# Kernel tuning notes

Measured on AMD Instinct MI355X. Metric: run time of the kernel, lower is better.

The kernel has to match this reference:

```python
import jax, jax.numpy as jnp
import numpy as np

B, L, E, H = 64, 512, 128, 256


def setup_inputs() -> dict:
    key = jax.random.key(0)
    ks = jax.random.split(key, 16)
    s = 0.05
    return {
        "embedded_inputs": jax.random.normal(ks[0], (B, L, E), jnp.float32),
        "decoder_input": jax.random.normal(ks[1], (B, E), jnp.float32),
        "h0": jax.random.normal(ks[2], (B, H), jnp.float32),
        "c0": jax.random.normal(ks[3], (B, H), jnp.float32),
        "context": jax.random.normal(ks[4], (B, L, H), jnp.float32),
        # LSTM cell params
        "Wi": jax.random.normal(ks[5], (4 * H, E), jnp.float32) * s,
        "bi": jnp.zeros((4 * H,), jnp.float32),
        "Wh": jax.random.normal(ks[6], (4 * H, H), jnp.float32) * s,
        "bh": jnp.zeros((4 * H,), jnp.float32),
        # hidden_out: Linear(2H -> H)
        "Wo": jax.random.normal(ks[7], (H, 2 * H), jnp.float32) * s,
        "bo": jnp.zeros((H,), jnp.float32),
        # attention params: input_linear(H->H), context conv1d(H->H,k=1), V [H]
        "Wa_in": jax.random.normal(ks[8], (H, H), jnp.float32) * s,
        "ba_in": jnp.zeros((H,), jnp.float32),
        "Wa_ctx": jax.random.normal(ks[9], (H, H), jnp.float32) * s,
        "ba_ctx": jnp.zeros((H,), jnp.float32),
        "V": jax.random.normal(ks[10], (H,), jnp.float32) * s,
    }


def reference(embedded_inputs, decoder_input, h0, c0, context,
              Wi, bi, Wh, bh, Wo, bo, Wa_in, ba_in, Wa_ctx, ba_ctx, V):
    # Precompute projected context once (Conv1d with kernel 1 == per-position linear): [B,L,H]
    ctx_proj = jnp.einsum('blh,gh->blg', context, Wa_ctx) + ba_ctx

    def step(carry, _):
        dec_in, h, c, mask = carry
        gates = dec_in @ Wi.T + bi + h @ Wh.T + bh              # [B,4H]
        i_g, f_g, g_g, o_g = jnp.split(gates, 4, axis=1)
        i_g = jax.nn.sigmoid(i_g)
        f_g = jax.nn.sigmoid(f_g)
        g_g = jnp.tanh(g_g)
        o_g = jax.nn.sigmoid(o_g)
        c_t = f_g * c + i_g * g_g
        h_t = o_g * jnp.tanh(c_t)
        # attention
        inp = h_t @ Wa_in.T + ba_in                              # [B,H]
        scores = jnp.einsum('h,blh->bl', V, jnp.tanh(inp[:, None, :] + ctx_proj))
        scores = jnp.where(mask == 0, -jnp.inf, scores)
        alpha = jax.nn.softmax(scores, axis=1)                   # [B,L]
        att_hidden = jnp.einsum('bl,blh->bh', alpha, ctx_proj)
        hidden_t = jnp.tanh(jnp.concatenate([att_hidden, h_t], axis=1) @ Wo.T + bo)
        # pointer: argmax over still-available positions
        masked_outs = alpha * mask
        idx = jnp.argmax(masked_outs, axis=1)                    # [B]
        one_hot = jax.nn.one_hot(idx, L, dtype=mask.dtype)
        mask_next = mask * (1.0 - one_hot)
        dec_next = jnp.take_along_axis(embedded_inputs, idx[:, None, None], axis=1)[:, 0]
        return (dec_next, hidden_t, c_t, mask_next), (alpha, idx)

    mask0 = jnp.ones((B, L), jnp.float32)
    carry0 = (decoder_input, h0, c0, mask0)
    (dec_f, h_f, c_f, _), (alphas, ptrs) = jax.lax.scan(step, carry0, None, length=L)
    outputs = jnp.transpose(alphas, (1, 0, 2))                   # [B,L,L]
    pointers = jnp.transpose(ptrs, (1, 0))                       # [B,L]
    return outputs, pointers, h_f, c_f
```

## Files before the change

kernel.cpp:

```cpp
#include <hip/hip_runtime.h>
#include <math.h>

#define SCOPE __HIP_MEMORY_SCOPE_AGENT

constexpr int Bn = 64, Ln = 512, En = 128, Hn = 256, Tn = 512;
constexpr int NBLK = 256, NTHR = 512;
constexpr int CTX_LD = 260;
constexpr int XPAD = 392, HTPAD = 264, UPAD = 520;

constexpr int OFF_CTX = 0;
constexpr int OFF_SCR = 128 * CTX_LD;
constexpr int OFF_HT  = OFF_SCR + 4096;
constexpr int OFF_INP = OFF_HT + 4 * HTPAD;
constexpr int OFF_SS  = OFF_INP + 256;
constexpr int OFF_ES  = OFF_SS + 128;
constexpr int OFF_MK  = OFF_ES + 128;
constexpr int OFF_VS  = OFF_MK + 128;
constexpr int OFF_ST  = OFF_VS + 256;
constexpr int OFF_WR  = OFF_ST + 64;
constexpr int OFF_X   = OFF_SCR;
constexpr int SMEM_FL = OFF_WR + 64;

constexpr size_t PTR_OFF = (size_t)Bn * Ln * Ln;
constexpr size_t HF_OFF  = PTR_OFF + (size_t)Bn * Ln;
constexpr size_t CF_OFF  = HF_OFF + (size_t)Bn * Hn;

constexpr int GQ_GATES = 0;
constexpr int GQ_INP   = 4096;
constexpr int GQ_ST    = 5120;
constexpr int GQ_ATT   = 5184;
constexpr int GQ_HID   = 9280;
constexpr int GQ_STRIDE = 10368;

__device__ __forceinline__ float fast_tanh(float x) {
  const float e = __expf(2.0f * x);
  return 1.0f - __fdividef(2.0f, 1.0f + e);
}
__device__ __forceinline__ float sigmoidf_(float x) {
  return 1.0f / (1.0f + expf(-x));
}
__device__ __forceinline__ void llc_storef(float* p, float v) {
  __hip_atomic_store(p, v, __ATOMIC_RELAXED, SCOPE);
}
__device__ __forceinline__ float llc_loadf(const float* p) {
  return __hip_atomic_load(p, __ATOMIC_RELAXED, SCOPE);
}
__device__ __forceinline__ unsigned long long llc_loadu64(const unsigned long long* p) {
  return __hip_atomic_load(p, __ATOMIC_RELAXED, SCOPE);
}

__device__ __forceinline__ void group_barrier16(unsigned* flags_g, int j, unsigned tgt) {
  asm volatile("s_waitcnt vmcnt(0)" ::: "memory");
  __syncthreads();
  if (threadIdx.x == 0)
    __hip_atomic_store(&flags_g[j * 32], tgt, __ATOMIC_RELAXED, SCOPE);
  if (threadIdx.x < 16) {
    long spins = 0;
    while (__hip_atomic_load(&flags_g[threadIdx.x * 32], __ATOMIC_RELAXED, SCOPE) < tgt) {
      __builtin_amdgcn_s_sleep(2);
      if (++spins > 50000000L) __builtin_trap();
    }
  }
  __syncthreads();
  asm volatile("" ::: "memory");
}

#define DOT4(acc, w4, x4) \
  acc = fmaf((w4).x, (x4).x, fmaf((w4).y, (x4).y, fmaf((w4).z, (x4).z, fmaf((w4).w, (x4).w, (acc)))))

__global__ void __launch_bounds__(NTHR, 2)
decoder_main(const float* __restrict__ emb, const float* __restrict__ dec0,
             const float* __restrict__ h0,  const float* __restrict__ c0,
             const float* __restrict__ ctxg,const float* __restrict__ Wi,
             const float* __restrict__ bi,  const float* __restrict__ Wh,
             const float* __restrict__ bh,  const float* __restrict__ Wo,
             const float* __restrict__ bo,  const float* __restrict__ Wain,
             const float* __restrict__ bain,const float* __restrict__ Wactx,
             const float* __restrict__ bactx,const float* __restrict__ Vv,
             float* __restrict__ out, unsigned* __restrict__ flags,
             float* __restrict__ wsd)
{
  extern __shared__ float sm[];
  float* ctx    = sm + OFF_CTX;
  float* scr    = sm + OFF_SCR;
  float* x_s    = sm + OFF_X;
  float* h_t_s  = sm + OFF_HT;
  float* inp_s  = sm + OFF_INP;
  float* s_s    = sm + OFF_SS;
  float* e_s    = sm + OFF_ES;
  float* mask_s = sm + OFF_MK;
  float* V_s    = sm + OFF_VS;
  float* stats_s= sm + OFF_ST;
  float* wred   = sm + OFF_WR;
  int*   wredi  = (int*)wred;

  const int tid = threadIdx.x, bid = blockIdx.x;
  const int gq = bid >> 4, j = bid & 15;
  const int bbj = j >> 2, ck = j & 3;
  const int b_ctx = gq * 4 + bbj;
  const int l0 = ck * 128;

  const int rloc = tid >> 3, seg8 = tid & 7;
  const int r_abs = j * 64 + rloc;
  const int r16loc = tid >> 5, seg32 = tid & 31;
  const int r16 = j * 16 + r16loc;

  unsigned* flags_g = flags + gq * (16 * 32);
  float* wsg = wsd + (size_t)gq * GQ_STRIDE;

  float4 wg4[12];
  #pragma unroll
  for (int k = 0; k < 12; ++k) {
    if (k < 4) wg4[k] = *(const float4*)&Wi[(size_t)r_abs * En + k * 32 + seg8 * 4];
    else       wg4[k] = *(const float4*)&Wh[(size_t)r_abs * Hn + (k - 4) * 32 + seg8 * 4];
  }
  const float bias_g = bi[r_abs] + bh[r_abs];
  float4 wa4[2];
  #pragma unroll
  for (int k = 0; k < 2; ++k) wa4[k] = *(const float4*)&Wain[(size_t)r16 * Hn + k * 128 + seg32 * 4];
  float4 wo4[4];
  #pragma unroll
  for (int k = 0; k < 4; ++k) wo4[k] = *(const float4*)&Wo[(size_t)r16 * (2 * Hn) + k * 128 + seg32 * 4];
  const float bain_r = bain[r16];
  const float bo_r = bo[r16];

  const int b2c = tid >> 7;
  const int hc = (2 * tid) & 255;
  float c0a = c0[(size_t)(gq * 4 + b2c) * Hn + hc];
  float c1a = c0[(size_t)(gq * 4 + b2c) * Hn + hc + 1];

  if (tid < 128) mask_s[tid] = 1.0f;
  if (tid < 256) V_s[tid] = Vv[tid];

  {
    const int gc = tid & 31, lg = tid >> 5;
    float acc[8][8];
    #pragma unroll
    for (int a2 = 0; a2 < 8; ++a2)
      #pragma unroll
      for (int b2 = 0; b2 < 8; ++b2) acc[a2][b2] = 0.0f;
    float* stg_c = scr;
    float* stg_w = scr + 1024;
    for (int kc = 0; kc < 32; ++kc) {
      __syncthreads();
      for (int i = tid; i < 1024; i += NTHR) {
        int k = i & 7, l = i >> 3;
        stg_c[k * 128 + l] = ctxg[((size_t)(b_ctx * Ln + l0 + l)) * Hn + kc * 8 + k];
      }
      for (int i = tid; i < 2048; i += NTHR) {
        int k = i & 7, gg = i >> 3;
        stg_w[k * 256 + gg] = Wactx[(size_t)gg * Hn + kc * 8 + k];
      }
      __syncthreads();
      #pragma unroll
      for (int kk = 0; kk < 8; ++kk) {
        float cl[8], wgt[8];
        #pragma unroll
        for (int jj = 0; jj < 8; ++jj) cl[jj] = stg_c[kk * 128 + lg * 8 + jj];
        #pragma unroll
        for (int jj = 0; jj < 8; ++jj) wgt[jj] = stg_w[kk * 256 + gc * 8 + jj];
        #pragma unroll
        for (int li = 0; li < 8; ++li)
          #pragma unroll
          for (int gi = 0; gi < 8; ++gi)
            acc[li][gi] = fmaf(cl[li], wgt[gi], acc[li][gi]);
      }
    }
    __syncthreads();
    #pragma unroll
    for (int li = 0; li < 8; ++li)
      #pragma unroll
      for (int gi = 0; gi < 8; ++gi)
        ctx[(lg * 8 + li) * CTX_LD + gc * 8 + gi] = acc[li][gi] + bactx[gc * 8 + gi];
  }
  __syncthreads();

  unsigned tgt = 1;
  int w0 = 0, w1 = 0, w2 = 0, w3 = 0;

  for (int t = 0; t < Tn; ++t) {
    {
      for (int i = tid; i < 4 * 384; i += NTHR) {
        const int bb = i / 384, c = i - bb * 384;
        const int gb = gq * 4 + bb;
        float v;
        if (c < 128) {
          if (t == 0) v = dec0[(size_t)gb * En + c];
          else {
            const int wsel = (bb == 0) ? w0 : (bb == 1) ? w1 : (bb == 2) ? w2 : w3;
            v = emb[((size_t)gb * Ln + wsel) * En + c];
          }
        } else {
          const int h = c - 128;
          v = (t == 0) ? h0[(size_t)gb * Hn + h]
                       : llc_loadf(wsg + GQ_HID + (h >> 4) * 64 + bb * 16 + (h & 15));
        }
        x_s[bb * XPAD + c] = v;
      }
      __syncthreads();
      #pragma unroll
      for (int bb = 0; bb < 4; ++bb) {
        float acc = 0.0f;
        #pragma unroll
        for (int k = 0; k < 12; ++k) {
          const float4 x4 = *(const float4*)&x_s[bb * XPAD + k * 32 + seg8 * 4];
          DOT4(acc, wg4[k], x4);
        }
        acc += __shfl_xor(acc, 1, 64);
        acc += __shfl_xor(acc, 2, 64);
        acc += __shfl_xor(acc, 4, 64);
        if (seg8 == 0)
          llc_storef(wsg + GQ_GATES + j * 256 + bb * 64 + rloc, acc + bias_g);
      }
    }
    group_barrier16(flags_g, j, tgt++);

    {
      unsigned long long* scr64 = (unsigned long long*)scr;
      const unsigned long long* src64 = (const unsigned long long*)(wsg + GQ_GATES);
      for (int i = tid; i < 2048; i += NTHR) scr64[i] = llc_loadu64(src64 + i);
      __syncthreads();
      {
        const int i0 = (hc >> 6) * 256 + b2c * 64 + (hc & 63);
        const float iv0 = scr[i0],        fv0 = scr[1024 + i0];
        const float gv0 = scr[2048 + i0], ov0 = scr[3072 + i0];
        const float iv1 = scr[i0 + 1],        fv1 = scr[1024 + i0 + 1];
        const float gv1 = scr[2048 + i0 + 1], ov1 = scr[3072 + i0 + 1];
        const float cn0 = sigmoidf_(fv0) * c0a + sigmoidf_(iv0) * tanhf(gv0);
        const float ht0 = sigmoidf_(ov0) * tanhf(cn0);
        const float cn1 = sigmoidf_(fv1) * c1a + sigmoidf_(iv1) * tanhf(gv1);
        const float ht1 = sigmoidf_(ov1) * tanhf(cn1);
        c0a = cn0; c1a = cn1;
        h_t_s[b2c * HTPAD + hc] = ht0;
        h_t_s[b2c * HTPAD + hc + 1] = ht1;
        if (t == Tn - 1 && j == 0) {
          out[CF_OFF + (size_t)(gq * 4 + b2c) * Hn + hc] = cn0;
          out[CF_OFF + (size_t)(gq * 4 + b2c) * Hn + hc + 1] = cn1;
        }
      }
      __syncthreads();
      #pragma unroll
      for (int bb = 0; bb < 4; ++bb) {
        float acc = 0.0f;
        #pragma unroll
        for (int k = 0; k < 2; ++k) {
          const float4 x4 = *(const float4*)&h_t_s[bb * HTPAD + k * 128 + seg32 * 4];
          DOT4(acc, wa4[k], x4);
        }
        acc += __shfl_xor(acc, 1, 64);
        acc += __shfl_xor(acc, 2, 64);
        acc += __shfl_xor(acc, 4, 64);
        acc += __shfl_xor(acc, 8, 64);
        acc += __shfl_xor(acc, 16, 64);
        if (seg32 == 0)
          llc_storef(wsg + GQ_INP + j * 64 + bb * 16 + r16loc, acc + bain_r);
      }
    }
    group_barrier16(flags_g, j, tgt++);

    {
      if (tid < 256)
        inp_s[tid] = llc_loadf(wsg + GQ_INP + (tid >> 4) * 64 + bbj * 16 + (tid & 15));
      __syncthreads();
      {
        const int l = tid >> 2, q = tid & 3;
        float p = 0.0f;
        #pragma unroll
        for (int i = 0; i < 16; ++i) {
          const int h4 = q * 64 + i * 4;
          const float4 c4 = *(const float4*)&ctx[l * CTX_LD + h4];
          const float4 in4 = *(const float4*)&inp_s[h4];
          const float4 v4 = *(const float4*)&V_s[h4];
          p = fmaf(v4.x, fast_tanh(in4.x + c4.x), p);
          p = fmaf(v4.y, fast_tanh(in4.y + c4.y), p);
          p = fmaf(v4.z, fast_tanh(in4.z + c4.z), p);
          p = fmaf(v4.w, fast_tanh(in4.w + c4.w), p);
        }
        p += __shfl_xor(p, 1, 64);
        p += __shfl_xor(p, 2, 64);
        if (q == 0) s_s[l] = (mask_s[l] == 0.0f) ? -INFINITY : p;
      }
      __syncthreads();
      if (tid < 128) {
        float v = s_s[tid];
        #pragma unroll
        for (int m = 1; m < 64; m <<= 1) v = fmaxf(v, __shfl_xor(v, m, 64));
        if ((tid & 63) == 0) wred[tid >> 6] = v;
      }
      __syncthreads();
      if (tid == 0) wred[2] = fmaxf(wred[0], wred[1]);
      __syncthreads();
      if (tid < 128) {
        const float mv = wred[2];
        const float sv = s_s[tid];
        const float e = (mask_s[tid] == 0.0f) ? 0.0f : expf(sv - mv);
        e_s[tid] = e;
        float ssum = e;
        #pragma unroll
        for (int m = 1; m < 64; m <<= 1) ssum += __shfl_xor(ssum, m, 64);
        float cv = sv; int ci = tid;
        #pragma unroll
        for (int m = 1; m < 64; m <<= 1) {
          const float ov = __shfl_xor(cv, m, 64);
          const int   oi = __shfl_xor(ci, m, 64);
          if (ov > cv || (ov == cv && oi < ci)) { cv = ov; ci = oi; }
        }
        if ((tid & 63) == 0) {
          wred[4 + (tid >> 6)] = ssum;
          wred[8 + (tid >> 6)] = cv;
          wredi[12 + (tid >> 6)] = ci;
        }
      }
      __syncthreads();
      if (tid == 0) {
        float bv = wred[8]; int bI = wredi[12];
        if (wred[9] > bv || (wred[9] == bv && wredi[13] < bI)) { bv = wred[9]; bI = wredi[13]; }
        float* stb = wsg + GQ_ST + (bbj * 4 + ck) * 4;
        llc_storef(stb + 0, wred[2]);
        llc_storef(stb + 1, wred[4] + wred[5]);
        llc_storef(stb + 2, bv);
        llc_storef(stb + 3, (float)(l0 + bI));
      }
      {
        const int h4g = tid & 63, lgq = tid >> 6;
        float p0 = 0, p1 = 0, p2 = 0, p3 = 0;
        #pragma unroll
        for (int li = 0; li < 16; ++li) {
          const int l = lgq * 16 + li;
          const float ev = e_s[l];
          const float4 c4 = *(const float4*)&ctx[l * CTX_LD + h4g * 4];
          p0 = fmaf(ev, c4.x, p0);
          p1 = fmaf(ev, c4.y, p1);
          p2 = fmaf(ev, c4.z, p2);
          p3 = fmaf(ev, c4.w, p3);
        }
        __syncthreads();
        *(float4*)&scr[lgq * 256 + h4g * 4] = make_float4(p0, p1, p2, p3);
      }
      __syncthreads();
      if (tid < 256) {
        float a = 0.0f;
        #pragma unroll
        for (int r2 = 0; r2 < 8; ++r2) a += scr[r2 * 256 + tid];
        llc_storef(wsg + GQ_ATT + (bbj * 4 + ck) * 256 + tid, a);
      }
    }
    group_barrier16(flags_g, j, tgt++);

    {
      if (tid < 64) stats_s[tid] = llc_loadf(wsg + GQ_ST + tid);
      __syncthreads();
      float Mb[4], Sb[4], sc[4][4];
      int wq[4];
      #pragma unroll
      for (int bb = 0; bb < 4; ++bb) {
        const float m0 = stats_s[(bb * 4 + 0) * 4], m1 = stats_s[(bb * 4 + 1) * 4];
        const float m2 = stats_s[(bb * 4 + 2) * 4], m3 = stats_s[(bb * 4 + 3) * 4];
        const float M = fmaxf(fmaxf(m0, m1), fmaxf(m2, m3));
        const float e0 = expf(m0 - M), e1 = expf(m1 - M);
        const float e2 = expf(m2 - M), e3 = expf(m3 - M);
        Mb[bb] = M;
        Sb[bb] = fmaf(e0, stats_s[(bb * 4 + 0) * 4 + 1],
                 fmaf(e1, stats_s[(bb * 4 + 1) * 4 + 1],
                 fmaf(e2, stats_s[(bb * 4 + 2) * 4 + 1],
                      e3 * stats_s[(bb * 4 + 3) * 4 + 1])));
        sc[bb][0] = e0; sc[bb][1] = e1; sc[bb][2] = e2; sc[bb][3] = e3;
        float bv = stats_s[(bb * 4 + 0) * 4 + 2];
        int bI = (int)stats_s[(bb * 4 + 0) * 4 + 3];
        #pragma unroll
        for (int c2 = 1; c2 < 4; ++c2) {
          const float v2 = stats_s[(bb * 4 + c2) * 4 + 2];
          const int i2 = (int)stats_s[(bb * 4 + c2) * 4 + 3];
          if (v2 > bv || (v2 == bv && i2 < bI)) { bv = v2; bI = i2; }
        }
        wq[bb] = bI;
      }
      float sck_own = 0, Stot_own = 0;
      int widx_own = 0;
      #pragma unroll
      for (int bb = 0; bb < 4; ++bb)
        if (bb == bbj) {
          Stot_own = Sb[bb]; widx_own = wq[bb];
          #pragma unroll
          for (int c2 = 0; c2 < 4; ++c2)
            if (c2 == ck) sck_own = sc[bb][c2];
        }
      if (tid < 128)
        out[(size_t)b_ctx * Ln * Ln + (size_t)t * Ln + l0 + tid] = e_s[tid] * (sck_own / Stot_own);
      if (tid == 0) {
        if (widx_own >= l0 && widx_own < l0 + 128) mask_s[widx_own - l0] = 0.0f;
        if (ck == 0) out[PTR_OFF + (size_t)b_ctx * Ln + t] = (float)widx_own;
      }
      #pragma unroll
      for (int bb = 0; bb < 4; ++bb) {
        float v;
        if (tid < 256) {
          const float a = fmaf(sc[bb][0], llc_loadf(wsg + GQ_ATT + (bb * 4 + 0) * 256 + tid),
                          fmaf(sc[bb][1], llc_loadf(wsg + GQ_ATT + (bb * 4 + 1) * 256 + tid),
                          fmaf(sc[bb][2], llc_loadf(wsg + GQ_ATT + (bb * 4 + 2) * 256 + tid),
                               sc[bb][3] * llc_loadf(wsg + GQ_ATT + (bb * 4 + 3) * 256 + tid))));
          v = a / Sb[bb];
        } else {
          v = h_t_s[bb * HTPAD + (tid - 256)];
        }
        scr[bb * UPAD + tid] = v;
      }
      __syncthreads();
      #pragma unroll
      for (int bb = 0; bb < 4; ++bb) {
        float acc = 0.0f;
        #pragma unroll
        for (int k = 0; k < 4; ++k) {
          const float4 x4 = *(const float4*)&scr[bb * UPAD + k * 128 + seg32 * 4];
          DOT4(acc, wo4[k], x4);
        }
        acc += __shfl_xor(acc, 1, 64);
        acc += __shfl_xor(acc, 2, 64);
        acc += __shfl_xor(acc, 4, 64);
        acc += __shfl_xor(acc, 8, 64);
        acc += __shfl_xor(acc, 16, 64);
        if (seg32 == 0) {
          const float hv = tanhf(acc + bo_r);
          llc_storef(wsg + GQ_HID + j * 64 + bb * 16 + r16loc, hv);
          if (t == Tn - 1) out[HF_OFF + (size_t)(gq * 4 + bb) * Hn + r16] = hv;
        }
      }
      w0 = wq[0]; w1 = wq[1]; w2 = wq[2]; w3 = wq[3];
    }
    group_barrier16(flags_g, j, tgt++);
  }
}

extern "C" void kernel_launch(void* const* d_in, const int* in_sizes, int n_in,
                              void* d_out, int out_size, void* d_ws, size_t ws_size,
                              hipStream_t stream) {
  (void)in_sizes; (void)n_in; (void)out_size; (void)ws_size;
  hipFuncSetAttribute(reinterpret_cast<const void*>(decoder_main),
                      hipFuncAttributeMaxDynamicSharedMemorySize, SMEM_FL * 4);
  hipMemsetAsync(d_ws, 0, 32768, stream);

  const float* emb   = (const float*)d_in[0];
  const float* dec0  = (const float*)d_in[1];
  const float* h0    = (const float*)d_in[2];
  const float* c0    = (const float*)d_in[3];
  const float* ctxg  = (const float*)d_in[4];
  const float* Wi    = (const float*)d_in[5];
  const float* bi    = (const float*)d_in[6];
  const float* Wh    = (const float*)d_in[7];
  const float* bh    = (const float*)d_in[8];
  const float* Wo    = (const float*)d_in[9];
  const float* bo    = (const float*)d_in[10];
  const float* Wain  = (const float*)d_in[11];
  const float* bain  = (const float*)d_in[12];
  const float* Wactx = (const float*)d_in[13];
  const float* bactx = (const float*)d_in[14];
  const float* V     = (const float*)d_in[15];

  unsigned* flags = (unsigned*)d_ws;
  float* wsd = (float*)((char*)d_ws + 32768);

  decoder_main<<<NBLK, NTHR, SMEM_FL * 4, stream>>>(
      emb, dec0, h0, c0, ctxg, Wi, bi, Wh, bh, Wo, bo, Wain, bain, Wactx, bactx, V,
      (float*)d_out, flags, wsd);
}
```

Baseline: 13.18 ms.

## Localize LSTM cell and attention input projection to drop one grid barrier per step

```diff
diff --git a/kernel.cpp b/kernel.cpp
--- a/kernel.cpp
+++ b/kernel.cpp
@@ -5,8 +5,7 @@
 
 constexpr int Bn = 64, Ln = 512, En = 128, Hn = 256, Tn = 512;
 constexpr int NBLK = 256, NTHR = 512;
-constexpr int CTX_LD = 260;
-constexpr int XPAD = 392, HTPAD = 264, UPAD = 520;
+constexpr int CTX_LD = 260, HTPAD = 264, XPAD = 384, UPAD = 520;
 
 constexpr int OFF_CTX = 0;
 constexpr int OFF_SCR = 128 * CTX_LD;
@@ -16,21 +15,20 @@
 constexpr int OFF_ES  = OFF_SS + 128;
 constexpr int OFF_MK  = OFF_ES + 128;
 constexpr int OFF_VS  = OFF_MK + 128;
-constexpr int OFF_ST  = OFF_VS + 256;
+constexpr int OFF_GS  = OFF_VS + 256;
+constexpr int OFF_ST  = OFF_GS + 256;
 constexpr int OFF_WR  = OFF_ST + 64;
-constexpr int OFF_X   = OFF_SCR;
 constexpr int SMEM_FL = OFF_WR + 64;
 
 constexpr size_t PTR_OFF = (size_t)Bn * Ln * Ln;
 constexpr size_t HF_OFF  = PTR_OFF + (size_t)Bn * Ln;
 constexpr size_t CF_OFF  = HF_OFF + (size_t)Bn * Hn;
 
-constexpr int GQ_GATES = 0;
-constexpr int GQ_INP   = 4096;
-constexpr int GQ_ST    = 5120;
-constexpr int GQ_ATT   = 5184;
-constexpr int GQ_HID   = 9280;
-constexpr int GQ_STRIDE = 10368;
+constexpr int GQ_HT    = 0;
+constexpr int GQ_HID   = 1024;
+constexpr int GQ_ATT   = 2048;
+constexpr int GQ_STATS = 6144;
+constexpr int GQ_STRIDE = 6208;
 
 __device__ __forceinline__ float fast_tanh(float x) {
   const float e = __expf(2.0f * x);
@@ -42,11 +40,23 @@
 __device__ __forceinline__ void llc_storef(float* p, float v) {
   __hip_atomic_store(p, v, __ATOMIC_RELAXED, SCOPE);
 }
-__device__ __forceinline__ float llc_loadf(const float* p) {
-  return __hip_atomic_load(p, __ATOMIC_RELAXED, SCOPE);
-}
-__device__ __forceinline__ unsigned long long llc_loadu64(const unsigned long long* p) {
-  return __hip_atomic_load(p, __ATOMIC_RELAXED, SCOPE);
+__device__ __forceinline__ float4 llc_ld4(const float* p) {
+  float4 r;
+  asm volatile("global_load_dwordx4 %0, %1, off sc0 sc1\n\ts_waitcnt vmcnt(0)"
+               : "=&v"(r) : "v"(p) : "memory");
+  return r;
+}
+__device__ __forceinline__ void llc_ld4x4(const float* p0, const float* p1,
+                                          const float* p2, const float* p3,
+                                          float4& a, float4& b, float4& c, float4& d) {
+  asm volatile(
+      "global_load_dwordx4 %0, %4, off sc0 sc1\n\t"
+      "global_load_dwordx4 %1, %5, off sc0 sc1\n\t"
+      "global_load_dwordx4 %2, %6, off sc0 sc1\n\t"
+      "global_load_dwordx4 %3, %7, off sc0 sc1\n\t"
+      "s_waitcnt vmcnt(0)"
+      : "=&v"(a), "=&v"(b), "=&v"(c), "=&v"(d)
+      : "v"(p0), "v"(p1), "v"(p2), "v"(p3) : "memory");
 }
 
 __device__ __forceinline__ void group_barrier16(unsigned* flags_g, int j, unsigned tgt) {
@@ -57,7 +67,7 @@
   if (threadIdx.x < 16) {
     long spins = 0;
     while (__hip_atomic_load(&flags_g[threadIdx.x * 32], __ATOMIC_RELAXED, SCOPE) < tgt) {
-      __builtin_amdgcn_s_sleep(2);
+      __builtin_amdgcn_s_sleep(1);
       if (++spins > 50000000L) __builtin_trap();
     }
   }
@@ -83,13 +93,14 @@
   extern __shared__ float sm[];
   float* ctx    = sm + OFF_CTX;
   float* scr    = sm + OFF_SCR;
-  float* x_s    = sm + OFF_X;
+  float* x_s    = sm + OFF_SCR;
   float* h_t_s  = sm + OFF_HT;
   float* inp_s  = sm + OFF_INP;
   float* s_s    = sm + OFF_SS;
   float* e_s    = sm + OFF_ES;
   float* mask_s = sm + OFF_MK;
   float* V_s    = sm + OFF_VS;
+  float* gsum   = sm + OFF_GS;
   float* stats_s= sm + OFF_ST;
   float* wred   = sm + OFF_WR;
   int*   wredi  = (int*)wred;
@@ -100,8 +111,10 @@
   const int b_ctx = gq * 4 + bbj;
   const int l0 = ck * 128;
 
-  const int rloc = tid >> 3, seg8 = tid & 7;
-  const int r_abs = j * 64 + rloc;
+  const int team = tid >> 3, seg8 = tid & 7;
+  const int gteam = team >> 4, hloc = team & 15;
+  const int r_abs = gteam * 256 + j * 16 + hloc;
+  const int irow = tid >> 1, ihalf = tid & 1;
   const int r16loc = tid >> 5, seg32 = tid & 31;
   const int r16 = j * 16 + r16loc;
 
@@ -110,24 +123,24 @@
 
   float4 wg4[12];
   #pragma unroll
-  for (int k = 0; k < 12; ++k) {
-    if (k < 4) wg4[k] = *(const float4*)&Wi[(size_t)r_abs * En + k * 32 + seg8 * 4];
-    else       wg4[k] = *(const float4*)&Wh[(size_t)r_abs * Hn + (k - 4) * 32 + seg8 * 4];
-  }
+  for (int k = 0; k < 4; ++k) wg4[k] = *(const float4*)&Wi[(size_t)r_abs * En + k * 32 + seg8 * 4];
+  #pragma unroll
+  for (int k = 0; k < 8; ++k) wg4[4 + k] = *(const float4*)&Wh[(size_t)r_abs * Hn + k * 32 + seg8 * 4];
   const float bias_g = bi[r_abs] + bh[r_abs];
-  float4 wa4[2];
+
+  float4 wn4[32];
   #pragma unroll
-  for (int k = 0; k < 2; ++k) wa4[k] = *(const float4*)&Wain[(size_t)r16 * Hn + k * 128 + seg32 * 4];
+  for (int k = 0; k < 32; ++k)
+    wn4[k] = *(const float4*)&Wain[(size_t)irow * Hn + ihalf * 128 + k * 4];
+  const float bain_r = bain[irow];
+
   float4 wo4[4];
   #pragma unroll
   for (int k = 0; k < 4; ++k) wo4[k] = *(const float4*)&Wo[(size_t)r16 * (2 * Hn) + k * 128 + seg32 * 4];
-  const float bain_r = bain[r16];
   const float bo_r = bo[r16];
 
-  const int b2c = tid >> 7;
-  const int hc = (2 * tid) & 255;
-  float c0a = c0[(size_t)(gq * 4 + b2c) * Hn + hc];
-  float c1a = c0[(size_t)(gq * 4 + b2c) * Hn + hc + 1];
+  float cst = 0.0f;
+  if (tid < 64) cst = c0[(size_t)(gq * 4 + (tid >> 4)) * Hn + j * 16 + (tid & 15)];
 
   if (tid < 128) mask_s[tid] = 1.0f;
   if (tid < 256) V_s[tid] = Vv[tid];
@@ -180,22 +193,22 @@
 
   for (int t = 0; t < Tn; ++t) {
     {
-      for (int i = tid; i < 4 * 384; i += NTHR) {
-        const int bb = i / 384, c = i - bb * 384;
-        const int gb = gq * 4 + bb;
-        float v;
-        if (c < 128) {
-          if (t == 0) v = dec0[(size_t)gb * En + c];
-          else {
-            const int wsel = (bb == 0) ? w0 : (bb == 1) ? w1 : (bb == 2) ? w2 : w3;
-            v = emb[((size_t)gb * Ln + wsel) * En + c];
-          }
-        } else {
-          const int h = c - 128;
-          v = (t == 0) ? h0[(size_t)gb * Hn + h]
-                       : llc_loadf(wsg + GQ_HID + (h >> 4) * 64 + bb * 16 + (h & 15));
-        }
-        x_s[bb * XPAD + c] = v;
+      if (tid < 256) {
+        const int bbx = tid >> 6, h4 = tid & 63;
+        float4 v;
+        if (t == 0) v = *(const float4*)&h0[(size_t)(gq * 4 + bbx) * Hn + h4 * 4];
+        else        v = llc_ld4(wsg + GQ_HID + bbx * 256 + h4 * 4);
+        *(float4*)&x_s[bbx * XPAD + 128 + h4 * 4] = v;
+      } else if (tid < 384) {
+        const int i2 = tid - 256, bbx = i2 >> 5, k4 = i2 & 31;
+        const int gb = gq * 4 + bbx;
+        float4 v;
+        if (t == 0) v = *(const float4*)&dec0[(size_t)gb * En + k4 * 4];
+        else {
+          const int wsel = (bbx == 0) ? w0 : (bbx == 1) ? w1 : (bbx == 2) ? w2 : w3;
+          v = *(const float4*)&emb[((size_t)gb * Ln + wsel) * En + k4 * 4];
+        }
+        *(float4*)&x_s[bbx * XPAD + k4 * 4] = v;
       }
       __syncthreads();
       #pragma unroll
@@ -209,58 +222,41 @@
         acc += __shfl_xor(acc, 1, 64);
         acc += __shfl_xor(acc, 2, 64);
         acc += __shfl_xor(acc, 4, 64);
-        if (seg8 == 0)
-          llc_storef(wsg + GQ_GATES + j * 256 + bb * 64 + rloc, acc + bias_g);
+        if (seg8 == 0) gsum[bb * 64 + team] = acc + bias_g;
+      }
+      __syncthreads();
+      if (tid < 64) {
+        const int bbx = tid >> 4, hx = tid & 15;
+        const float iv = gsum[bbx * 64 + hx];
+        const float fv = gsum[bbx * 64 + 16 + hx];
+        const float gv = gsum[bbx * 64 + 32 + hx];
+        const float ov = gsum[bbx * 64 + 48 + hx];
+        const float cn = sigmoidf_(fv) * cst + sigmoidf_(iv) * tanhf(gv);
+        const float htv = sigmoidf_(ov) * tanhf(cn);
+        cst = cn;
+        llc_storef(wsg + GQ_HT + bbx * 256 + j * 16 + hx, htv);
+        if (t == Tn - 1) out[CF_OFF + (size_t)(gq * 4 + bbx) * Hn + j * 16 + hx] = cn;
       }
     }
     group_barrier16(flags_g, j, tgt++);
 
     {
-      unsigned long long* scr64 = (unsigned long long*)scr;
-      const unsigned long long* src64 = (const unsigned long long*)(wsg + GQ_GATES);
-      for (int i = tid; i < 2048; i += NTHR) scr64[i] = llc_loadu64(src64 + i);
+      if (tid < 256) {
+        const int bbx = tid >> 6, h4 = tid & 63;
+        const float4 v = llc_ld4(wsg + GQ_HT + tid * 4);
+        *(float4*)&h_t_s[bbx * HTPAD + h4 * 4] = v;
+      }
       __syncthreads();
       {
-        const int i0 = (hc >> 6) * 256 + b2c * 64 + (hc & 63);
-        const float iv0 = scr[i0],        fv0 = scr[1024 + i0];
-        const float gv0 = scr[2048 + i0], ov0 = scr[3072 + i0];
-        const float iv1 = scr[i0 + 1],        fv1 = scr[1024 + i0 + 1];
-        const float gv1 = scr[2048 + i0 + 1], ov1 = scr[3072 + i0 + 1];
-        const float cn0 = sigmoidf_(fv0) * c0a + sigmoidf_(iv0) * tanhf(gv0);
-        const float ht0 = sigmoidf_(ov0) * tanhf(cn0);
-        const float cn1 = sigmoidf_(fv1) * c1a + sigmoidf_(iv1) * tanhf(gv1);
-        const float ht1 = sigmoidf_(ov1) * tanhf(cn1);
-        c0a = cn0; c1a = cn1;
-        h_t_s[b2c * HTPAD + hc] = ht0;
-        h_t_s[b2c * HTPAD + hc + 1] = ht1;
-        if (t == Tn - 1 && j == 0) {
-          out[CF_OFF + (size_t)(gq * 4 + b2c) * Hn + hc] = cn0;
-          out[CF_OFF + (size_t)(gq * 4 + b2c) * Hn + hc + 1] = cn1;
-        }
-      }
-      __syncthreads();
-      #pragma unroll
-      for (int bb = 0; bb < 4; ++bb) {
         float acc = 0.0f;
         #pragma unroll
-        for (int k = 0; k < 2; ++k) {
-          const float4 x4 = *(const float4*)&h_t_s[bb * HTPAD + k * 128 + seg32 * 4];
-          DOT4(acc, wa4[k], x4);
+        for (int k = 0; k < 32; ++k) {
+          const float4 x4 = *(const float4*)&h_t_s[bbj * HTPAD + ihalf * 128 + k * 4];
+          DOT4(acc, wn4[k], x4);
         }
         acc += __shfl_xor(acc, 1, 64);
-        acc += __shfl_xor(acc, 2, 64);
-        acc += __shfl_xor(acc, 4, 64);
-        acc += __shfl_xor(acc, 8, 64);
-        acc += __shfl_xor(acc, 16, 64);
-        if (seg32 == 0)
-          llc_storef(wsg + GQ_INP + j * 64 + bb * 16 + r16loc, acc + bain_r);
-      }
-    }
-    group_barrier16(flags_g, j, tgt++);
-
-    {
-      if (tid < 256)
-        inp_s[tid] = llc_loadf(wsg + GQ_INP + (tid >> 4) * 64 + bbj * 16 + (tid & 15));
+        if (ihalf == 0) inp_s[irow] = acc + bain_r;
+      }
       __syncthreads();
       {
         const int l = tid >> 2, q = tid & 3;
@@ -282,18 +278,8 @@
       }
       __syncthreads();
       if (tid < 128) {
-        float v = s_s[tid];
-        #pragma unroll
-        for (int m = 1; m < 64; m <<= 1) v = fmaxf(v, __shfl_xor(v, m, 64));
-        if ((tid & 63) == 0) wred[tid >> 6] = v;
-      }
-      __syncthreads();
-      if (tid == 0) wred[2] = fmaxf(wred[0], wred[1]);
-      __syncthreads();
-      if (tid < 128) {
-        const float mv = wred[2];
         const float sv = s_s[tid];
-        const float e = (mask_s[tid] == 0.0f) ? 0.0f : expf(sv - mv);
+        const float e = expf(sv);
         e_s[tid] = e;
         float ssum = e;
         #pragma unroll
@@ -306,20 +292,20 @@
           if (ov > cv || (ov == cv && oi < ci)) { cv = ov; ci = oi; }
         }
         if ((tid & 63) == 0) {
-          wred[4 + (tid >> 6)] = ssum;
-          wred[8 + (tid >> 6)] = cv;
-          wredi[12 + (tid >> 6)] = ci;
+          wred[tid >> 6] = ssum;
+          wred[4 + (tid >> 6)] = cv;
+          wredi[8 + (tid >> 6)] = ci;
         }
       }
       __syncthreads();
       if (tid == 0) {
-        float bv = wred[8]; int bI = wredi[12];
-        if (wred[9] > bv || (wred[9] == bv && wredi[13] < bI)) { bv = wred[9]; bI = wredi[13]; }
-        float* stb = wsg + GQ_ST + (bbj * 4 + ck) * 4;
-        llc_storef(stb + 0, wred[2]);
-        llc_storef(stb + 1, wred[4] + wred[5]);
-        llc_storef(stb + 2, bv);
-        llc_storef(stb + 3, (float)(l0 + bI));
+        const float S = wred[0] + wred[1];
+        float bv = wred[4]; int bI = wredi[8];
+        if (wred[5] > bv || (wred[5] == bv && wredi[9] < bI)) { bv = wred[5]; bI = wredi[9]; }
+        float* stb = wsg + GQ_STATS + (bbj * 4 + ck) * 4;
+        llc_storef(stb + 0, S);
+        llc_storef(stb + 1, bv);
+        llc_storef(stb + 2, (float)(l0 + bI));
       }
       {
         const int h4g = tid & 63, lgq = tid >> 6;
@@ -334,7 +320,6 @@
           p2 = fmaf(ev, c4.z, p2);
           p3 = fmaf(ev, c4.w, p3);
         }
-        __syncthreads();
         *(float4*)&scr[lgq * 256 + h4g * 4] = make_float4(p0, p1, p2, p3);
       }
       __syncthreads();
@@ -348,62 +333,53 @@
     group_barrier16(flags_g, j, tgt++);
 
     {
-      if (tid < 64) stats_s[tid] = llc_loadf(wsg + GQ_ST + tid);
-      __syncthreads();
-      float Mb[4], Sb[4], sc[4][4];
-      int wq[4];
+      if (tid < 16) {
+        const float4 st = llc_ld4(wsg + GQ_STATS + tid * 4);
+        *(float4*)&stats_s[tid * 4] = st;
+      }
+      __syncthreads();
+      float Sb[4]; int wq[4];
       #pragma unroll
       for (int bb = 0; bb < 4; ++bb) {
-        const float m0 = stats_s[(bb * 4 + 0) * 4], m1 = stats_s[(bb * 4 + 1) * 4];
-        const float m2 = stats_s[(bb * 4 + 2) * 4], m3 = stats_s[(bb * 4 + 3) * 4];
-        const float M = fmaxf(fmaxf(m0, m1), fmaxf(m2, m3));
-        const float e0 = expf(m0 - M), e1 = expf(m1 - M);
-        const float e2 = expf(m2 - M), e3 = expf(m3 - M);
-        Mb[bb] = M;
-        Sb[bb] = fmaf(e0, stats_s[(bb * 4 + 0) * 4 + 1],
-                 fmaf(e1, stats_s[(bb * 4 + 1) * 4 + 1],
-                 fmaf(e2, stats_s[(bb * 4 + 2) * 4 + 1],
-                      e3 * stats_s[(bb * 4 + 3) * 4 + 1])));
-        sc[bb][0] = e0; sc[bb][1] = e1; sc[bb][2] = e2; sc[bb][3] = e3;
-        float bv = stats_s[(bb * 4 + 0) * 4 + 2];
-        int bI = (int)stats_s[(bb * 4 + 0) * 4 + 3];
+        Sb[bb] = ((stats_s[(bb * 4 + 0) * 4] + stats_s[(bb * 4 + 1) * 4])
+                  + stats_s[(bb * 4 + 2) * 4]) + stats_s[(bb * 4 + 3) * 4];
+        float bv = stats_s[(bb * 4 + 0) * 4 + 1];
+        int bI = (int)stats_s[(bb * 4 + 0) * 4 + 2];
         #pragma unroll
         for (int c2 = 1; c2 < 4; ++c2) {
-          const float v2 = stats_s[(bb * 4 + c2) * 4 + 2];
-          const int i2 = (int)stats_s[(bb * 4 + c2) * 4 + 3];
+          const float v2 = stats_s[(bb * 4 + c2) * 4 + 1];
+          const int i2 = (int)stats_s[(bb * 4 + c2) * 4 + 2];
           if (v2 > bv || (v2 == bv && i2 < bI)) { bv = v2; bI = i2; }
         }
         wq[bb] = bI;
       }
-      float sck_own = 0, Stot_own = 0;
-      int widx_own = 0;
-      #pragma unroll
-      for (int bb = 0; bb < 4; ++bb)
-        if (bb == bbj) {
-          Stot_own = Sb[bb]; widx_own = wq[bb];
-          #pragma unroll
-          for (int c2 = 0; c2 < 4; ++c2)
-            if (c2 == ck) sck_own = sc[bb][c2];
-        }
-      if (tid < 128)
-        out[(size_t)b_ctx * Ln * Ln + (size_t)t * Ln + l0 + tid] = e_s[tid] * (sck_own / Stot_own);
+      const float Sown = (bbj == 0) ? Sb[0] : (bbj == 1) ? Sb[1] : (bbj == 2) ? Sb[2] : Sb[3];
+      const int wown = (bbj == 0) ? wq[0] : (bbj == 1) ? wq[1] : (bbj == 2) ? wq[2] : wq[3];
+      if (tid < 32) {
+        const float4 e4 = *(const float4*)&e_s[tid * 4];
+        *(float4*)&out[(size_t)b_ctx * Ln * Ln + (size_t)t * Ln + l0 + tid * 4] =
+            make_float4(e4.x / Sown, e4.y / Sown, e4.z / Sown, e4.w / Sown);
+      }
       if (tid == 0) {
-        if (widx_own >= l0 && widx_own < l0 + 128) mask_s[widx_own - l0] = 0.0f;
-        if (ck == 0) out[PTR_OFF + (size_t)b_ctx * Ln + t] = (float)widx_own;
-      }
-      #pragma unroll
-      for (int bb = 0; bb < 4; ++bb) {
-        float v;
-        if (tid < 256) {
-          const float a = fmaf(sc[bb][0], llc_loadf(wsg + GQ_ATT + (bb * 4 + 0) * 256 + tid),
-                          fmaf(sc[bb][1], llc_loadf(wsg + GQ_ATT + (bb * 4 + 1) * 256 + tid),
-                          fmaf(sc[bb][2], llc_loadf(wsg + GQ_ATT + (bb * 4 + 2) * 256 + tid),
-                               sc[bb][3] * llc_loadf(wsg + GQ_ATT + (bb * 4 + 3) * 256 + tid))));
-          v = a / Sb[bb];
-        } else {
-          v = h_t_s[bb * HTPAD + (tid - 256)];
-        }
-        scr[bb * UPAD + tid] = v;
+        if (wown >= l0 && wown < l0 + 128) mask_s[wown - l0] = 0.0f;
+        if (ck == 0) out[PTR_OFF + (size_t)b_ctx * Ln + t] = (float)wown;
+      }
+      if (tid < 256) {
+        const int bbx = tid >> 6, h4 = tid & 63;
+        const float* ab = wsg + GQ_ATT + bbx * 4 * 256 + h4 * 4;
+        float4 a0, a1, a2, a3;
+        llc_ld4x4(ab, ab + 256, ab + 512, ab + 768, a0, a1, a2, a3);
+        const float Sx = (bbx == 0) ? Sb[0] : (bbx == 1) ? Sb[1] : (bbx == 2) ? Sb[2] : Sb[3];
+        float4 u4;
+        u4.x = (((a0.x + a1.x) + a2.x) + a3.x) / Sx;
+        u4.y = (((a0.y + a1.y) + a2.y) + a3.y) / Sx;
+        u4.z = (((a0.z + a1.z) + a2.z) + a3.z) / Sx;
+        u4.w = (((a0.w + a1.w) + a2.w) + a3.w) / Sx;
+        *(float4*)&scr[bbx * UPAD + h4 * 4] = u4;
+      } else {
+        const int i2 = tid - 256, bbx = i2 >> 6, h4 = i2 & 63;
+        const float4 hv = *(const float4*)&h_t_s[bbx * HTPAD + h4 * 4];
+        *(float4*)&scr[bbx * UPAD + 256 + h4 * 4] = hv;
       }
       __syncthreads();
       #pragma unroll
@@ -421,7 +397,7 @@
         acc += __shfl_xor(acc, 16, 64);
         if (seg32 == 0) {
           const float hv = tanhf(acc + bo_r);
-          llc_storef(wsg + GQ_HID + j * 64 + bb * 16 + r16loc, hv);
+          llc_storef(wsg + GQ_HID + bb * 256 + r16, hv);
           if (t == Tn - 1) out[HF_OFF + (size_t)(gq * 4 + bb) * Hn + r16] = hv;
         }
       }
@@ -435,9 +411,9 @@
                               void* d_out, int out_size, void* d_ws, size_t ws_size,
                               hipStream_t stream) {
   (void)in_sizes; (void)n_in; (void)out_size; (void)ws_size;
-  hipFuncSetAttribute(reinterpret_cast<const void*>(decoder_main),
-                      hipFuncAttributeMaxDynamicSharedMemorySize, SMEM_FL * 4);
-  hipMemsetAsync(d_ws, 0, 32768, stream);
+  (void)hipFuncSetAttribute(reinterpret_cast<const void*>(decoder_main),
+                            hipFuncAttributeMaxDynamicSharedMemorySize, SMEM_FL * 4);
+  (void)hipMemsetAsync(d_ws, 0, 32768, stream);
 
   const float* emb   = (const float*)d_in[0];
   const float* dec0  = (const float*)d_in[1];
```

New measurement: 13.40 ms. No clear change (+1.7%).
